# Kernel optimization log

Hardware: AMD Instinct MI355X
Metric: run time of the kernel (lower is better)

Reference implementation:

```python
import jax, jax.numpy as jnp
import numpy as np

DIM = 1024
N_HEAD = 16
SEQ = 2048
GATE_IN = 12
ROPE_BASE = 10000.0
ATTN_SCALE = 0.1
EPS = 1e-6


def setup_inputs() -> dict:
    key = jax.random.key(0)
    ks = jax.random.split(key, 8)
    std = 0.5 * DIM ** -0.5
    bound = (3.0 ** 0.5) * std
    x = jax.random.normal(ks[0], (1, SEQ, DIM), dtype=jnp.float32)
    v1 = jax.random.normal(ks[1], (1, SEQ, DIM), dtype=jnp.float32)
    Wq = jax.random.uniform(ks[2], (DIM, DIM), jnp.float32, -bound, bound)
    Wk = jax.random.uniform(ks[3], (DIM, DIM), jnp.float32, -bound, bound)
    Wv = jax.random.uniform(ks[4], (DIM, DIM), jnp.float32, -bound, bound)
    # original zero-inits c_proj/attn_gate; use small random so output is non-trivial
    Wproj = jax.random.normal(ks[5], (DIM, DIM), dtype=jnp.float32) * 0.02
    Wgate = jax.random.normal(ks[6], (N_HEAD, GATE_IN), dtype=jnp.float32) * 0.02
    lamb = jnp.float32(0.5)
    return {"x": x, "v1": v1, "Wq": Wq, "Wk": Wk, "Wv": Wv,
            "Wproj": Wproj, "lamb": lamb, "Wgate": Wgate}


def _rms_norm(t):
    return t * jax.lax.rsqrt(jnp.mean(jnp.square(t), axis=-1, keepdims=True) + EPS)


def _rotary(t):
    # t: [B, T, H, hd]; rotates halves per the module's sign convention
    B, T, H, hd = t.shape
    d = hd // 2
    inv_freq = 1.0 / (ROPE_BASE ** (jnp.arange(0, hd, 2, dtype=jnp.float32) / hd))  # [d]
    freqs = jnp.arange(T, dtype=jnp.float32)[:, None] * inv_freq[None, :]  # [T, d]
    cos = jnp.cos(freqs)[None, :, None, :]
    sin = jnp.sin(freqs)[None, :, None, :]
    x1, x2 = t[..., :d], t[..., d:]
    y1 = x1 * cos + x2 * sin
    y2 = -x1 * sin + x2 * cos
    return jnp.concatenate([y1, y2], axis=-1)


def reference(x, v1, Wq, Wk, Wv, Wproj, lamb, Wgate):
    B, T, dim = x.shape
    H = Wgate.shape[0]
    hd = dim // H

    q = (x @ Wq.T).reshape(B, T, H, hd)
    k = (x @ Wk.T).reshape(B, T, H, hd)
    v = (x @ Wv.T).reshape(B, T, H, hd)

    # lambda-blended value mixing with residual value stream v1
    v = (1.0 - lamb) * v + lamb * v1.reshape(B, T, H, hd)

    q, k = _rms_norm(q), _rms_norm(k)
    q, k = _rotary(q), _rotary(k)

    # causal attention with fixed scale 0.1 (flex_attention block-sparse causal)
    scores = jnp.einsum("bthd,bshd->bhts", q, k) * ATTN_SCALE  # [B,H,T,T]
    causal = jnp.tril(jnp.ones((T, T), dtype=bool))
    scores = jnp.where(causal[None, None], scores, jnp.float32(-1e30))
    probs = jax.nn.softmax(scores, axis=-1)
    y = jnp.einsum("bhts,bshd->bthd", probs, v)  # [B,T,H,hd]

    # sigmoid gate from the first 12 channels of x, per head
    gate = jax.nn.sigmoid(x[..., :Wgate.shape[1]] @ Wgate.T)[..., None]  # [B,T,H,1]
    y = (y * gate).reshape(B, T, dim)
    y = y @ Wproj.T
    return y, v1
```

## Files before the change

kernel.cpp:

```cpp
#include <hip/hip_runtime.h>
#include <hip/hip_bf16.h>

#define T_SEQ 2048
#define NH 16
#define HD 64
#define SCALE_LOG2E 0.14426950408889634f

typedef __attribute__((ext_vector_type(8))) short bf16x8;
typedef __attribute__((ext_vector_type(4))) short bf16x4;
typedef __attribute__((ext_vector_type(4))) float f32x4;

__device__ __forceinline__ short f2bs(float f) {
  union { float f; unsigned u; } v; v.f = f;
  unsigned r = v.u + 0x7fffu + ((v.u >> 16) & 1u);
  return (short)(r >> 16);
}

__device__ __forceinline__ float bs2f(short s) {
  union { unsigned u; float f; } v;
  v.u = ((unsigned)(unsigned short)s) << 16;
  return v.f;
}

__device__ __forceinline__ unsigned cvt_pk_bf16(float lo, float hi) {
  unsigned r;
  asm("v_cvt_pk_bf16_f32 %0, %1, %2" : "=v"(r) : "v"(lo), "v"(hi));
  return r;
}

__device__ __forceinline__ void gload16(const short* g, short* l) {
  __builtin_amdgcn_global_load_lds(
      (const __attribute__((address_space(1))) void*)g,
      (__attribute__((address_space(3))) void*)l, 16, 0, 0);
}

__global__ __launch_bounds__(256) void prep(const float* __restrict__ x,
                                            const float* __restrict__ wq,
                                            const float* __restrict__ wk,
                                            const float* __restrict__ wv,
                                            const float* __restrict__ wp,
                                            const float* __restrict__ v1,
                                            const float* __restrict__ Wg,
                                            short* __restrict__ xbT,
                                            short* __restrict__ wqkvT,
                                            short* __restrict__ wpjT,
                                            float* __restrict__ out2,
                                            float* __restrict__ gate,
                                            float2* __restrict__ rope) {
  const int rt = blockIdx.x;
  const int tid = threadIdx.x;
  if (blockIdx.y == 8) {
    int id = rt * 256 + tid;
    int t = id >> 4, h = id & 15;
    float acc = 0.f;
    #pragma unroll
    for (int i = 0; i < 12; ++i) acc += x[(size_t)t * 1024 + i] * Wg[h * 12 + i];
    gate[id] = 1.f / (1.f + __expf(-acc));
    #pragma unroll
    for (int j = 0; j < 2; ++j) {
      int e = id * 2 + j;
      int tt = e >> 5, p = e & 31;
      float invf = __builtin_exp2f(-0.41524101186092f * (float)p);
      float s, c;
      sincosf((float)tt * invf, &s, &c);
      rope[e] = make_float2(c, s);
    }
    return;
  }
  if (rt >= 96) {
    const int r0 = (rt - 96) * 64;
    const float* s = v1 + (size_t)r0 * 1024 + blockIdx.y * 128;
    float* d = out2 + (size_t)r0 * 1024 + blockIdx.y * 128;
    #pragma unroll
    for (int it = 0; it < 8; ++it) {
      int e = it * 256 + tid;
      int r = e >> 5, c4 = e & 31;
      *(float4*)&d[(size_t)r * 1024 + c4 * 4] = *(const float4*)&s[(size_t)r * 1024 + c4 * 4];
    }
    return;
  }
  __shared__ __attribute__((aligned(16))) short lv[64][136];
  const float* src; short* dst; int srow0, drow0, R;
  if (rt < 32)      { src = x;  dst = xbT;   R = 2048; srow0 = rt * 64;        drow0 = srow0; }
  else if (rt < 48) { src = wq; dst = wqkvT; R = 3072; srow0 = (rt - 32) * 64; drow0 = srow0; }
  else if (rt < 64) { src = wk; dst = wqkvT; R = 3072; srow0 = (rt - 48) * 64; drow0 = srow0 + 1024; }
  else if (rt < 80) { src = wv; dst = wqkvT; R = 3072; srow0 = (rt - 64) * 64; drow0 = srow0 + 2048; }
  else              { src = wp; dst = wpjT;  R = 1024; srow0 = (rt - 80) * 64; drow0 = srow0; }
  const int c0 = blockIdx.y * 16;
  #pragma unroll
  for (int it = 0; it < 8; ++it) {
    int e = it * 256 + tid;
    int r = e >> 5, c4 = e & 31;
    float4 v = *(const float4*)&src[(size_t)(srow0 + r) * 1024 + blockIdx.y * 128 + c4 * 4];
    bf16x4 o; o[0] = f2bs(v.x); o[1] = f2bs(v.y); o[2] = f2bs(v.z); o[3] = f2bs(v.w);
    *(bf16x4*)&lv[r][c4 * 4] = o;
  }
  __syncthreads();
  #pragma unroll
  for (int it = 0; it < 4; ++it) {
    int e = it * 256 + tid;
    int kc = e >> 6, r = e & 63;
    bf16x8 w = *(const bf16x8*)&lv[r][kc * 8];
    *(bf16x8*)&dst[((size_t)(c0 + kc) * R + drow0 + r) * 8] = w;
  }
}

template <int BM, bool QKV>
__global__ __launch_bounds__(256) void gemm(const short* __restrict__ A,
                                            const short* __restrict__ B,
                                            float* __restrict__ C,
                                            short* __restrict__ qb,
                                            short* __restrict__ kb,
                                            short* __restrict__ vt,
                                            const float* __restrict__ v1,
                                            const float* __restrict__ lambp,
                                            const float2* __restrict__ rope,
                                            int M, int N, int K) {
  constexpr int MF = BM / 32;
  constexpr int LA = BM / 64;
  __shared__ union {
    struct { short As[3][4][BM][8]; short Bs[3][4][128][8]; } g;
    short lv[128][130];
  } sm;
  const int tid = threadIdx.x;
  const int lane = tid & 63, wid = tid >> 6;
  const int lr = lane & 15, lg = lane >> 4;
  const int wm = (wid >> 1) * (BM / 2), wn = (wid & 1) * 64;
  const int bm = blockIdx.x * BM, bn = blockIdx.y * 128;
  const short* Ap = A + ((size_t)wid * M + bm + lane) * 8;
  const short* Bp = B + ((size_t)wid * N + bn + lane) * 8;
  f32x4 acc[MF][4] = {};
  auto stage = [&](int buf, int k0) {
    #pragma unroll
    for (int g = 0; g < LA; ++g)
      gload16(Ap + (size_t)k0 * M + g * 512, &sm.g.As[buf][wid][64 * g][0]);
    gload16(Bp + (size_t)k0 * N,       &sm.g.Bs[buf][wid][0][0]);
    gload16(Bp + (size_t)k0 * N + 512, &sm.g.Bs[buf][wid][64][0]);
  };
  auto compute = [&](int buf) {
    bf16x8 af[MF], bfr[4];
    #pragma unroll
    for (int m = 0; m < MF; ++m) af[m] = *(const bf16x8*)&sm.g.As[buf][lg][wm + m * 16 + lr][0];
    #pragma unroll
    for (int n = 0; n < 4; ++n) bfr[n] = *(const bf16x8*)&sm.g.Bs[buf][lg][wn + n * 16 + lr][0];
    #pragma unroll
    for (int m = 0; m < MF; ++m)
      #pragma unroll
      for (int n = 0; n < 4; ++n)
        acc[m][n] = __builtin_amdgcn_mfma_f32_16x16x32_bf16(af[m], bfr[n], acc[m][n], 0, 0, 0);
  };
  const int nsteps = K >> 5;
  stage(0, 0);
  stage(1, 32);
  int cur = 0;
  for (int ks = 0; ks < nsteps - 1; ++ks) {
    if constexpr (BM == 128) asm volatile("s_waitcnt vmcnt(4)" ::: "memory");
    else                     asm volatile("s_waitcnt vmcnt(3)" ::: "memory");
    __builtin_amdgcn_s_barrier();
    __builtin_amdgcn_sched_barrier(0);
    int s2 = cur + 2; if (s2 >= 3) s2 -= 3;
    if (ks + 2 < nsteps) stage(s2, (ks + 2) * 32);
    compute(cur);
    cur = (cur == 2) ? 0 : cur + 1;
  }
  asm volatile("s_waitcnt vmcnt(0)" ::: "memory");
  __builtin_amdgcn_s_barrier();
  __builtin_amdgcn_sched_barrier(0);
  compute(cur);

  if constexpr (QKV) {
    if (bn < 2048) {
      const bool isq = (bn < 1024);
      short* dst = isq ? qb : kb;
      const int h = ((bn + wn) & 1023) >> 6;
      #pragma unroll
      for (int m = 0; m < MF; ++m)
        #pragma unroll
        for (int r = 0; r < 4; ++r) {
          const int t = bm + wm + m * 16 + 4 * lg + r;
          float ss = acc[m][0][r] * acc[m][0][r] + acc[m][1][r] * acc[m][1][r]
                   + acc[m][2][r] * acc[m][2][r] + acc[m][3][r] * acc[m][3][r];
          ss += __shfl_xor(ss, 1);
          ss += __shfl_xor(ss, 2);
          ss += __shfl_xor(ss, 4);
          ss += __shfl_xor(ss, 8);
          const float rms = rsqrtf(ss * (1.f / 64.f) + 1e-6f);
          short* row = dst + ((size_t)h * T_SEQ + t) * 64;
          #pragma unroll
          for (int n2 = 0; n2 < 2; ++n2) {
            float x1 = acc[m][n2][r] * rms, x2 = acc[m][n2 + 2][r] * rms;
            float2 cs = rope[t * 32 + n2 * 16 + lr];
            float y1 = x1 * cs.x + x2 * cs.y;
            float y2 = x2 * cs.x - x1 * cs.y;
            if (isq) { y1 *= SCALE_LOG2E; y2 *= SCALE_LOG2E; }
            row[n2 * 16 + lr] = f2bs(y1);
            row[32 + n2 * 16 + lr] = f2bs(y2);
          }
        }
    } else {
      const float Lb = *lambp;
      const int h0 = (bn - 2048) >> 6;
      __syncthreads();
      #pragma unroll
      for (int m = 0; m < MF; ++m)
        #pragma unroll
        for (int r = 0; r < 4; ++r) {
          const int tl = wm + m * 16 + 4 * lg + r;
          const size_t vrow = (size_t)(bm + tl) * 1024 + h0 * 64;
          #pragma unroll
          for (int n = 0; n < 4; ++n) {
            const int col = wn + n * 16 + lr;
            float w = v1[vrow + col];
            sm.lv[tl][col] = f2bs((1.f - Lb) * acc[m][n][r] + Lb * w);
          }
        }
      __syncthreads();
      #pragma unroll
      for (int it = 0; it < 8; ++it) {
        int u = it * 256 + tid;
        int c0 = (u & 15) * 8;
        int d = (u >> 4) & 63;
        int hh = u >> 10;
        bf16x8 w;
        #pragma unroll
        for (int j = 0; j < 8; ++j) {
          int c = c0 + j;
          int src = (c & 96) | ((c & 1) << 4) | ((c >> 1) & 15);
          w[j] = sm.lv[src][hh * 64 + d];
        }
        *(bf16x8*)&vt[((size_t)(h0 + hh) * 64 + d) * T_SEQ + bm + c0] = w;
      }
    }
  } else {
    #pragma unroll
    for (int m = 0; m < MF; ++m)
      #pragma unroll
      for (int r = 0; r < 4; ++r) {
        const int t = bm + wm + m * 16 + 4 * lg + r;
        float* Cr = C + (size_t)t * N + bn + wn + lr;
        #pragma unroll
        for (int n = 0; n < 4; ++n) Cr[n * 16] = acc[m][n][r];
      }
  }
}

__global__ __launch_bounds__(256) void attn(const short* __restrict__ qb,
                                            const short* __restrict__ kb,
                                            const short* __restrict__ vtp,
                                            short* __restrict__ partO,
                                            float* __restrict__ partL) {
  __shared__ __attribute__((aligned(16))) short Ks[2][4096];
  __shared__ __attribute__((aligned(16))) short Vs[2][4096];
  __shared__ __attribute__((aligned(16))) short p_lds[4][16][72];
  const int head = blockIdx.x & 15;
  const int b = blockIdx.x >> 4;
  int strip, qg;
  if (b < 32)      { strip = 0; qg = 31 - b; }
  else if (b < 56) { strip = 1; qg = 63 - b; }
  else if (b < 72) { strip = 2; qg = 87 - b; }
  else             { strip = 3; qg = 103 - b; }
  const int nt = min(8, qg + 1 - strip * 8);
  const int lane = threadIdx.x & 63, wid = threadIdx.x >> 6;
  const int lr = lane & 15, lg = lane >> 4;
  const int qt0 = qg * 64 + wid * 16;
  const short* Q = qb + (size_t)head * (T_SEQ * HD);
  const short* Kp = kb + (size_t)head * (T_SEQ * HD);
  const short* Vt = vtp + (size_t)head * (HD * T_SEQ);
  short (*P)[72] = p_lds[wid];

  bf16x8 aq0 = *(const bf16x8*)&Q[(size_t)(qt0 + lr) * HD + 8 * lg];
  bf16x8 aq1 = *(const bf16x8*)&Q[(size_t)(qt0 + lr) * HD + 32 + 8 * lg];
  f32x4 accO[4] = {};
  float lsum[4] = {0.f, 0.f, 0.f, 0.f};

  auto stage = [&](int buf, int jg) {
    const int kv0 = jg * 64;
    #pragma unroll
    for (int i = 0; i < 2; ++i) {
      int s = i * 256 + wid * 64 + lane;
      int row = s >> 3;
      int cG = (s & 7) ^ (row & 7);
      gload16(Kp + (size_t)(kv0 + row) * HD + cG * 8,
              &Ks[buf][(size_t)(i * 256 + wid * 64) * 8]);
      gload16(Vt + (size_t)row * T_SEQ + kv0 + cG * 8,
              &Vs[buf][(size_t)(i * 256 + wid * 64) * 8]);
    }
  };
  stage(0, strip * 8);
  for (int j = 0; j < nt; ++j) {
    const int jg = strip * 8 + j;
    __syncthreads();
    if (j + 1 < nt) stage((j + 1) & 1, jg + 1);
    const short* Kb = Ks[j & 1];
    const short* Vb = Vs[j & 1];
    f32x4 st[4];
    #pragma unroll
    for (int t = 0; t < 4; ++t) {
      int row = 16 * t + lr;
      int c0 = lg ^ (row & 7);
      bf16x8 k0 = *(const bf16x8*)&Kb[row * 64 + c0 * 8];
      bf16x8 k1 = *(const bf16x8*)&Kb[row * 64 + (c0 ^ 4) * 8];
      f32x4 s = {};
      s = __builtin_amdgcn_mfma_f32_16x16x32_bf16(aq0, k0, s, 0, 0, 0);
      s = __builtin_amdgcn_mfma_f32_16x16x32_bf16(aq1, k1, s, 0, 0, 0);
      st[t] = s;
    }
    if (jg == qg) {
      #pragma unroll
      for (int t = 0; t < 4; ++t)
        #pragma unroll
        for (int r = 0; r < 4; ++r)
          st[t][r] = (16 * t + lr > wid * 16 + 4 * lg + r) ? -1e30f : st[t][r];
    }
    #pragma unroll
    for (int r = 0; r < 4; ++r) {
      float p0 = __builtin_exp2f(st[0][r]);
      float p1 = __builtin_exp2f(st[1][r]);
      float p2 = __builtin_exp2f(st[2][r]);
      float p3 = __builtin_exp2f(st[3][r]);
      lsum[r] += (p0 + p1) + (p2 + p3);
      *(unsigned*)&P[4 * lg + r][2 * lr] = cvt_pk_bf16(p0, p1);
      *(unsigned*)&P[4 * lg + r][32 + 2 * lr] = cvt_pk_bf16(p2, p3);
    }
    asm volatile("s_waitcnt lgkmcnt(0)" ::: "memory");
    __builtin_amdgcn_sched_barrier(0);
    bf16x8 pa0 = *(const bf16x8*)&P[lr][8 * lg];
    bf16x8 pa1 = *(const bf16x8*)&P[lr][32 + 8 * lg];
    #pragma unroll
    for (int nv = 0; nv < 4; ++nv) {
      int row0 = nv * 16 + lr;
      int c0 = lg ^ (row0 & 7);
      bf16x8 v0 = *(const bf16x8*)&Vb[row0 * 64 + c0 * 8];
      bf16x8 v1e = *(const bf16x8*)&Vb[row0 * 64 + (c0 ^ 4) * 8];
      accO[nv] = __builtin_amdgcn_mfma_f32_16x16x32_bf16(pa0, v0, accO[nv], 0, 0, 0);
      accO[nv] = __builtin_amdgcn_mfma_f32_16x16x32_bf16(pa1, v1e, accO[nv], 0, 0, 0);
    }
  }
  short* pO = partO + (size_t)(head * 80 + b) * 4096;
  float* pL = partL + (size_t)(head * 80 + b) * 64;
  #pragma unroll
  for (int r = 0; r < 4; ++r) {
    float sres = lsum[r];
    sres += __shfl_xor(sres, 1);
    sres += __shfl_xor(sres, 2);
    sres += __shfl_xor(sres, 4);
    sres += __shfl_xor(sres, 8);
    int row = wid * 16 + 4 * lg + r;
    #pragma unroll
    for (int nv = 0; nv < 4; ++nv)
      pO[row * 64 + nv * 16 + lr] = f2bs(accO[nv][r]);
    if (lr == 0) pL[row] = sres;
  }
}

__global__ __launch_bounds__(256) void attn_reduce(const short* __restrict__ partO,
                                                   const float* __restrict__ partL,
                                                   const float* __restrict__ gate,
                                                   short* __restrict__ obT) {
  const int head = blockIdx.x & 15;
  const int qg = blockIdx.x >> 4;
  const int ns = (qg >> 3) + 1;
  const int tid = threadIdx.x;
  const int row = tid >> 2, q4 = tid & 3;
  const int sbase[4] = {0, 32, 56, 72};
  f32x4 o[4] = {};
  float l = 0.f;
  for (int s = 0; s < ns; ++s) {
    const int slot = head * 80 + sbase[s] + 31 - qg;
    const short* pb = partO + (size_t)slot * 4096;
    #pragma unroll
    for (int c = 0; c < 4; ++c) {
      bf16x4 v = *(const bf16x4*)&pb[row * 64 + q4 * 16 + c * 4];
      #pragma unroll
      for (int j = 0; j < 4; ++j) o[c][j] += bs2f(v[j]);
    }
    l += partL[(size_t)slot * 64 + row];
  }
  const int t = qg * 64 + row;
  const float gs = gate[t * 16 + head] / l;
  const int cg0 = head * 8 + q4 * 2;
  bf16x8 w0, w1;
  #pragma unroll
  for (int j = 0; j < 4; ++j) {
    w0[j]     = f2bs(o[0][j] * gs);
    w0[4 + j] = f2bs(o[1][j] * gs);
    w1[j]     = f2bs(o[2][j] * gs);
    w1[4 + j] = f2bs(o[3][j] * gs);
  }
  *(bf16x8*)&obT[((size_t)cg0 * 2048 + t) * 8] = w0;
  *(bf16x8*)&obT[((size_t)(cg0 + 1) * 2048 + t) * 8] = w1;
}

extern "C" void kernel_launch(void* const* d_in, const int* in_sizes, int n_in,
                              void* d_out, int out_size, void* d_ws, size_t ws_size,
                              hipStream_t stream) {
  const float* x     = (const float*)d_in[0];
  const float* v1    = (const float*)d_in[1];
  const float* Wq    = (const float*)d_in[2];
  const float* Wk    = (const float*)d_in[3];
  const float* Wv    = (const float*)d_in[4];
  const float* Wproj = (const float*)d_in[5];
  const float* lamb  = (const float*)d_in[6];
  const float* Wgate = (const float*)d_in[7];
  float* out = (float*)d_out;

  char* ws = (char*)d_ws;
  short*  xbT   = (short*)(ws);
  short*  wqkvT = (short*)(ws + ((size_t)4  << 20));
  short*  wpjT  = (short*)(ws + ((size_t)10 << 20));
  short*  partO = (short*)(ws + ((size_t)12 << 20));
  float*  partL = (float*)(ws + ((size_t)23 << 20));
  float2* rope  = (float2*)(ws + ((size_t)34 << 20));
  short*  qb    = (short*)(ws + ((size_t)36 << 20));
  short*  kb    = (short*)(ws + ((size_t)40 << 20));
  short*  vt    = (short*)(ws + ((size_t)44 << 20));
  float*  gate  = (float*)(ws + ((size_t)48 << 20));
  short*  obT   = xbT;

  prep<<<dim3(128, 9), 256, 0, stream>>>(x, Wq, Wk, Wv, Wproj, v1, Wgate,
                                         xbT, wqkvT, wpjT,
                                         out + (size_t)T_SEQ * 1024, gate, rope);
  gemm<128, true><<<dim3(16, 24), 256, 0, stream>>>(xbT, wqkvT, nullptr, qb, kb, vt,
                                                    v1, lamb, rope, 2048, 3072, 1024);
  attn<<<1280, 256, 0, stream>>>(qb, kb, vt, partO, partL);
  attn_reduce<<<512, 256, 0, stream>>>(partO, partL, gate, obT);
  gemm<64, false><<<dim3(32, 8), 256, 0, stream>>>(obT, wpjT, out, nullptr, nullptr,
                                                   nullptr, nullptr, nullptr, nullptr,
                                                   2048, 1024, 1024);
}
```

Measured before the change: 75.70 us.

## Shrink GEMM tiles and remap blocks for XCD-aware scheduling

The GEMM kernel now takes a BN template parameter and uses smaller tiles: 64x128 for the QKV projection (768 blocks) and 64x64 for the output projection (512 blocks). It also switches to a 1D grid whose block index is remapped so that consecutive tiles land on the same XCD (blockIdx & 7 interleave). Both changes aim to fill the 256 CUs better and improve L2 locality. In exchange, each block gets less data reuse per tile and the V transpose epilogue is adjusted for the smaller BM.

Measured after the change: 73.31 us. 1.03x faster.

```diff
diff --git a/kernel.cpp b/kernel.cpp
--- a/kernel.cpp
+++ b/kernel.cpp
@@ -105,7 +105,7 @@
   }
 }
 
-template <int BM, bool QKV>
+template <int BM, int BN, bool QKV>
 __global__ __launch_bounds__(256) void gemm(const short* __restrict__ A,
                                             const short* __restrict__ B,
                                             float* __restrict__ C,
@@ -116,37 +116,41 @@
                                             const float* __restrict__ lambp,
                                             const float2* __restrict__ rope,
                                             int M, int N, int K) {
-  constexpr int MF = BM / 32;
-  constexpr int LA = BM / 64;
+  constexpr int MF = BM / 32, NB = BN / 32;
+  constexpr int LA = BM / 64, LB = BN / 64;
   __shared__ union {
-    struct { short As[3][4][BM][8]; short Bs[3][4][128][8]; } g;
-    short lv[128][130];
+    struct { short As[3][4][BM][8]; short Bs[3][4][BN][8]; } g;
+    short lv[BM][130];
   } sm;
   const int tid = threadIdx.x;
   const int lane = tid & 63, wid = tid >> 6;
   const int lr = lane & 15, lg = lane >> 4;
-  const int wm = (wid >> 1) * (BM / 2), wn = (wid & 1) * 64;
-  const int bm = blockIdx.x * BM, bn = blockIdx.y * 128;
+  const int wm = (wid >> 1) * (BM / 2), wn = (wid & 1) * (BN / 2);
+  const int nper = gridDim.x >> 3;
+  const int tile = (blockIdx.x & 7) * nper + (blockIdx.x >> 3);
+  const int gx = M / BM;
+  const int bm = (tile % gx) * BM, bn = (tile / gx) * BN;
   const short* Ap = A + ((size_t)wid * M + bm + lane) * 8;
   const short* Bp = B + ((size_t)wid * N + bn + lane) * 8;
-  f32x4 acc[MF][4] = {};
+  f32x4 acc[MF][NB] = {};
   auto stage = [&](int buf, int k0) {
     #pragma unroll
     for (int g = 0; g < LA; ++g)
       gload16(Ap + (size_t)k0 * M + g * 512, &sm.g.As[buf][wid][64 * g][0]);
-    gload16(Bp + (size_t)k0 * N,       &sm.g.Bs[buf][wid][0][0]);
-    gload16(Bp + (size_t)k0 * N + 512, &sm.g.Bs[buf][wid][64][0]);
+    #pragma unroll
+    for (int g = 0; g < LB; ++g)
+      gload16(Bp + (size_t)k0 * N + g * 512, &sm.g.Bs[buf][wid][64 * g][0]);
   };
   auto compute = [&](int buf) {
-    bf16x8 af[MF], bfr[4];
+    bf16x8 af[MF], bfr[NB];
     #pragma unroll
     for (int m = 0; m < MF; ++m) af[m] = *(const bf16x8*)&sm.g.As[buf][lg][wm + m * 16 + lr][0];
     #pragma unroll
-    for (int n = 0; n < 4; ++n) bfr[n] = *(const bf16x8*)&sm.g.Bs[buf][lg][wn + n * 16 + lr][0];
+    for (int n = 0; n < NB; ++n) bfr[n] = *(const bf16x8*)&sm.g.Bs[buf][lg][wn + n * 16 + lr][0];
     #pragma unroll
     for (int m = 0; m < MF; ++m)
       #pragma unroll
-      for (int n = 0; n < 4; ++n)
+      for (int n = 0; n < NB; ++n)
         acc[m][n] = __builtin_amdgcn_mfma_f32_16x16x32_bf16(af[m], bfr[n], acc[m][n], 0, 0, 0);
   };
   const int nsteps = K >> 5;
@@ -154,8 +158,9 @@
   stage(1, 32);
   int cur = 0;
   for (int ks = 0; ks < nsteps - 1; ++ks) {
-    if constexpr (BM == 128) asm volatile("s_waitcnt vmcnt(4)" ::: "memory");
-    else                     asm volatile("s_waitcnt vmcnt(3)" ::: "memory");
+    if constexpr (LA + LB == 4)      asm volatile("s_waitcnt vmcnt(4)" ::: "memory");
+    else if constexpr (LA + LB == 3) asm volatile("s_waitcnt vmcnt(3)" ::: "memory");
+    else                             asm volatile("s_waitcnt vmcnt(2)" ::: "memory");
     __builtin_amdgcn_s_barrier();
     __builtin_amdgcn_sched_barrier(0);
     int s2 = cur + 2; if (s2 >= 3) s2 -= 3;
@@ -208,19 +213,20 @@
           const int tl = wm + m * 16 + 4 * lg + r;
           const size_t vrow = (size_t)(bm + tl) * 1024 + h0 * 64;
           #pragma unroll
-          for (int n = 0; n < 4; ++n) {
+          for (int n = 0; n < NB; ++n) {
             const int col = wn + n * 16 + lr;
             float w = v1[vrow + col];
             sm.lv[tl][col] = f2bs((1.f - Lb) * acc[m][n][r] + Lb * w);
           }
         }
       __syncthreads();
-      #pragma unroll
-      for (int it = 0; it < 8; ++it) {
+      constexpr int TPB = BM / 8;
+      #pragma unroll
+      for (int it = 0; it < BM / 16; ++it) {
         int u = it * 256 + tid;
-        int c0 = (u & 15) * 8;
-        int d = (u >> 4) & 63;
-        int hh = u >> 10;
+        int c0 = (u % TPB) * 8;
+        int d = (u / TPB) & 63;
+        int hh = u / (TPB * 64);
         bf16x8 w;
         #pragma unroll
         for (int j = 0; j < 8; ++j) {
@@ -239,7 +245,7 @@
         const int t = bm + wm + m * 16 + 4 * lg + r;
         float* Cr = C + (size_t)t * N + bn + wn + lr;
         #pragma unroll
-        for (int n = 0; n < 4; ++n) Cr[n * 16] = acc[m][n][r];
+        for (int n = 0; n < NB; ++n) Cr[n * 16] = acc[m][n][r];
       }
   }
 }
@@ -420,11 +426,11 @@
   prep<<<dim3(128, 9), 256, 0, stream>>>(x, Wq, Wk, Wv, Wproj, v1, Wgate,
                                          xbT, wqkvT, wpjT,
                                          out + (size_t)T_SEQ * 1024, gate, rope);
-  gemm<128, true><<<dim3(16, 24), 256, 0, stream>>>(xbT, wqkvT, nullptr, qb, kb, vt,
-                                                    v1, lamb, rope, 2048, 3072, 1024);
+  gemm<64, 128, true><<<768, 256, 0, stream>>>(xbT, wqkvT, nullptr, qb, kb, vt,
+                                               v1, lamb, rope, 2048, 3072, 1024);
   attn<<<1280, 256, 0, stream>>>(qb, kb, vt, partO, partL);
   attn_reduce<<<512, 256, 0, stream>>>(partO, partL, gate, obT);
-  gemm<64, false><<<dim3(32, 8), 256, 0, stream>>>(obT, wpjT, out, nullptr, nullptr,
-                                                   nullptr, nullptr, nullptr, nullptr,
-                                                   2048, 1024, 1024);
-}
+  gemm<64, 64, false><<<512, 256, 0, stream>>>(obT, wpjT, out, nullptr, nullptr,
+                                               nullptr, nullptr, nullptr, nullptr,
+                                               2048, 1024, 1024);
+}
```
